# Performance work log

Measured on AMD Instinct MI355X. Metric: run time of the kernel, lower is better.

## Reference

```python
import jax, jax.numpy as jnp
import numpy as np

N = 100000   # nodes
E = 1600000  # edges (avg degree 16)
IN, HID, OUT = 128, 128, 64
EPS = 1e-5


def setup_inputs() -> dict:
    key = jax.random.key(0)
    ks = jax.random.split(key, 8)
    x = jax.random.normal(ks[0], (N, IN), dtype=jnp.float32)
    edge_index = jax.random.randint(ks[1], (2, E), 0, N, dtype=jnp.int64)

    def w(k, i, o):
        return jax.random.normal(k, (i, o), dtype=jnp.float32) / np.float32(np.sqrt(i))

    return {
        'x': x,
        'edge_index': edge_index,
        'W1': w(ks[2], IN, HID), 'b1': jnp.zeros((HID,), jnp.float32),
        'g1': jnp.ones((HID,), jnp.float32), 'be1': jnp.zeros((HID,), jnp.float32),
        'W2': w(ks[3], HID, HID), 'b2': jnp.zeros((HID,), jnp.float32),
        'g2': jnp.ones((HID,), jnp.float32), 'be2': jnp.zeros((HID,), jnp.float32),
        'W3': w(ks[4], HID, OUT), 'b3': jnp.zeros((OUT,), jnp.float32),
    }


def gcn_conv(x, W, b, src, dst, n):
    # GCNConv: x' = D^{-1/2} (A + I) D^{-1/2} X W + b
    h = x @ W                                   # [N, F_out]
    loop = jnp.arange(n, dtype=src.dtype)
    s = jnp.concatenate([src, loop])            # self-loops appended
    d = jnp.concatenate([dst, loop])
    deg = jax.ops.segment_sum(jnp.ones_like(d, dtype=h.dtype), d, num_segments=n)
    dinv = jax.lax.rsqrt(jnp.maximum(deg, 1.0))  # deg >= 1 due to self-loops
    norm = dinv[s] * dinv[d]                     # [E+N]
    out = jax.ops.segment_sum(h[s] * norm[:, None], d, num_segments=n)
    return out + b


def batch_norm(x, gamma, beta):
    m = x.mean(axis=0)
    v = x.var(axis=0)  # biased variance, as used for normalization in torch BN
    return (x - m) * jax.lax.rsqrt(v + EPS) * gamma + beta


def reference(x, edge_index, W1, b1, g1, be1, W2, b2, g2, be2, W3, b3):
    src, dst = edge_index[0], edge_index[1]
    r = x                                        # residual (skip = Identity, in_dim == hidden_dim)
    h = batch_norm(gcn_conv(x, W1, b1, src, dst, N), g1, be1) + r
    r = h
    h = jax.nn.relu(h)                           # dropout p=0 -> identity
    h = batch_norm(gcn_conv(h, W2, b2, src, dst, N), g2, be2) + r
    h = jax.nn.relu(h)
    out = gcn_conv(h, W3, b3, src, dst, N)       # last layer: no bn/skip/relu
    return out
```

## Files before the change

### kernel.cpp

```cpp
#include <hip/hip_runtime.h>

static constexpr int kN = 100000;
static constexpr int kE = 1600000;
static constexpr float kEps = 1e-5f;

static constexpr int kBSH = 9;
static constexpr int kNB = (kN + 511) >> kBSH;
static constexpr int kBCAP = 12288;
static constexpr int kCHUNK = 4096;
static constexpr int kPad = 16;

typedef __attribute__((ext_vector_type(8))) short short8;
typedef __attribute__((ext_vector_type(4))) float float4v;
typedef __attribute__((ext_vector_type(2))) float float2v;

static __device__ inline unsigned short f2bf(float f) {
  union { float f; unsigned int u; } v; v.f = f;
  unsigned int r = v.u + 0x7fffu + ((v.u >> 16) & 1u);
  return (unsigned short)(r >> 16);
}
static __device__ inline float bf2f(unsigned int bits16) {
  union { unsigned int u; float f; } v; v.u = bits16 << 16; return v.f;
}
static __device__ inline unsigned int pack2bf(float lo, float hi) {
  return (unsigned int)f2bf(lo) | ((unsigned int)f2bf(hi) << 16);
}

__global__ __launch_bounds__(512) void bin_k(const int* __restrict__ src,
                                             const int* __restrict__ dst,
                                             int* __restrict__ gcursor,
                                             int2* __restrict__ gstage) {
  __shared__ int s_cnt[256];
  __shared__ int s_scan[256];
  __shared__ int s_base[256];
  __shared__ int s_cur[256];
  __shared__ int s_gb[256];
  __shared__ int2 s_stage[kCHUNK];
  int tid = threadIdx.x;
  int e0 = blockIdx.x * kCHUNK;
  int n = kE - e0; if (n > kCHUNK) n = kCHUNK;
  if (tid < 256) s_cnt[tid] = 0;
  __syncthreads();
  for (int j = tid; j < n; j += 512) {
    atomicAdd(&s_cnt[dst[e0 + j] >> kBSH], 1);
  }
  __syncthreads();
  int v = 0;
  if (tid < 256) { v = s_cnt[tid]; s_scan[tid] = v; }
  __syncthreads();
  #pragma unroll
  for (int o = 1; o < 256; o <<= 1) {
    int t = (tid >= o && tid < 256) ? s_scan[tid - o] : 0;
    __syncthreads();
    if (tid < 256) s_scan[tid] += t;
    __syncthreads();
  }
  if (tid < 256) {
    int excl = s_scan[tid] - v;
    s_base[tid] = excl;
    s_cur[tid] = excl;
  }
  __syncthreads();
  if (tid < kNB && s_cnt[tid] > 0) s_gb[tid] = atomicAdd(&gcursor[tid], s_cnt[tid]);
  for (int j = tid; j < n; j += 512) {
    int s = src[e0 + j];
    int d = dst[e0 + j];
    int p = atomicAdd(&s_cur[d >> kBSH], 1);
    s_stage[p] = make_int2(s, d);
  }
  __syncthreads();
  for (int j = tid; j < n; j += 512) {
    int2 e = s_stage[j];
    int b = e.y >> kBSH;
    gstage[(size_t)b * kBCAP + s_gb[b] + (j - s_base[b])] = e;
  }
}

__global__ __launch_bounds__(256) void alloc_hist_k(const int2* __restrict__ gstage,
                                                    const int* __restrict__ gcursor,
                                                    int* __restrict__ counter,
                                                    int* __restrict__ deg,
                                                    int* __restrict__ row_start,
                                                    float* __restrict__ dinv) {
  __shared__ int s_deg[1 << kBSH];
  __shared__ int s_scan[256];
  __shared__ int s_bcast;
  int b = blockIdx.x, tid = threadIdx.x;
  int n0 = b << kBSH;
  s_deg[tid] = 0;
  s_deg[tid + 256] = 0;
  __syncthreads();
  int cnt = gcursor[b];
  const int2* seg = gstage + (size_t)b * kBCAP;
  for (int j = tid; j < cnt; j += 256) {
    atomicAdd(&s_deg[seg[j].y - n0], 1);
  }
  __syncthreads();
  int i0 = 2 * tid, i1 = 2 * tid + 1;
  int d0 = s_deg[i0], d1 = s_deg[i1];
  int pd0 = (d0 + kPad - 1) & ~(kPad - 1);
  int pd1 = (d1 + kPad - 1) & ~(kPad - 1);
  int sum = pd0 + pd1;
  s_scan[tid] = sum;
  __syncthreads();
  #pragma unroll
  for (int o = 1; o < 256; o <<= 1) {
    int t = (tid >= o) ? s_scan[tid - o] : 0;
    __syncthreads();
    s_scan[tid] += t;
    __syncthreads();
  }
  if (tid == 255) s_bcast = atomicAdd(counter, s_scan[255]);
  __syncthreads();
  int base = s_bcast + s_scan[tid] - sum;
  int node0 = n0 + i0, node1 = n0 + i1;
  if (node0 < kN) {
    deg[node0] = d0;
    row_start[node0] = base;
    dinv[node0] = rsqrtf((float)(d0 + 1));
  }
  if (node1 < kN) {
    deg[node1] = d1;
    row_start[node1] = base + pd0;
    dinv[node1] = rsqrtf((float)(d1 + 1));
  }
}

__global__ __launch_bounds__(256) void scatter2_k(const int2* __restrict__ gstage,
                                                  const int* __restrict__ gcursor,
                                                  const int* __restrict__ rowst,
                                                  const int* __restrict__ deg,
                                                  int* __restrict__ csr_src) {
  __shared__ int s_cur[1 << kBSH];
  int b = blockIdx.x, tid = threadIdx.x;
  int n0 = b << kBSH;
  int nn = kN - n0; if (nn > (1 << kBSH)) nn = 1 << kBSH;
  for (int i = tid; i < nn; i += 256) s_cur[i] = rowst[n0 + i];
  __syncthreads();
  int cnt = gcursor[b];
  const int2* seg = gstage + (size_t)b * kBCAP;
  for (int j = tid; j < cnt; j += 256) {
    int2 e = seg[j];
    int pos = atomicAdd(&s_cur[e.y - n0], 1);
    csr_src[pos] = e.x;
  }
  __syncthreads();
  for (int i = tid; i < nn; i += 256) {
    int d = deg[n0 + i];
    int endp = rowst[n0 + i] + ((d + kPad - 1) & ~(kPad - 1));
    for (int p = s_cur[i]; p < endp; ++p) csr_src[p] = kN;
  }
}

__global__ void convert_w_all_k(const float* __restrict__ W1, const float* __restrict__ W2,
                                const float* __restrict__ W3,
                                unsigned short* __restrict__ wf1,
                                unsigned short* __restrict__ wf2,
                                unsigned short* __restrict__ wf3,
                                unsigned char* __restrict__ hF8,
                                unsigned short* __restrict__ hH) {
  int tid = blockIdx.x * blockDim.x + threadIdx.x;
  const float* W;
  unsigned short* Wf;
  int BNO;
  if (tid < 2048) { W = W1; Wf = wf1; BNO = 128; }
  else if (tid < 4096) { W = W2; Wf = wf2; BNO = 128; tid -= 2048; }
  else if (tid < 5120) { W = W3; Wf = wf3; BNO = 64; tid -= 4096; }
  else if (tid < 5152) {
    ((unsigned int*)(hF8 + (size_t)kN * 128))[tid - 5120] = 0u;
    return;
  } else if (tid < 5184) {
    ((unsigned int*)(hH + (size_t)kN * 64))[tid - 5152] = 0u;
    return;
  } else return;
  int l = tid & 63;
  int frag = tid >> 6;
  int q = frag & 3;
  int t = frag >> 2;
  int n = t * 16 + (l & 15);
  int kbase = q * 32 + ((l >> 4) << 3);
  unsigned short v[8] __attribute__((aligned(16)));
  #pragma unroll
  for (int j = 0; j < 8; ++j) v[j] = f2bf(W[(kbase + j) * BNO + n]);
  ((uint4*)Wf)[tid] = *(const uint4*)v;
}

template <int BNO, bool AF32, bool OUT8>
__global__ __launch_bounds__(256) void gemm_mfma_k(const void* __restrict__ Aptr,
                                                   const unsigned short* __restrict__ Wf,
                                                   const float* __restrict__ dinv,
                                                   void* __restrict__ Cptr,
                                                   float* __restrict__ stats) {
  if (stats && blockIdx.x == 0) stats[threadIdx.x] = 0.f;
  int wid = (int)((blockIdx.x * blockDim.x + threadIdx.x) >> 6);
  if (wid >= kN / 16) return;
  int l = threadIdx.x & 63;
  int r0 = wid * 16;
  short8 a[4];
  if constexpr (AF32) {
    const float* Af = (const float*)Aptr + (size_t)(r0 + (l & 15)) * 128 + ((l >> 4) << 3);
    #pragma unroll
    for (int q = 0; q < 4; ++q) {
      float4 u0 = *(const float4*)(Af + q * 32);
      float4 u1 = *(const float4*)(Af + q * 32 + 4);
      short8 t;
      t[0] = (short)f2bf(u0.x); t[1] = (short)f2bf(u0.y);
      t[2] = (short)f2bf(u0.z); t[3] = (short)f2bf(u0.w);
      t[4] = (short)f2bf(u1.x); t[5] = (short)f2bf(u1.y);
      t[6] = (short)f2bf(u1.z); t[7] = (short)f2bf(u1.w);
      a[q] = t;
    }
  } else {
    const short8* Arow =
        (const short8*)((const unsigned short*)Aptr + (size_t)(r0 + (l & 15)) * 128 + ((l >> 4) << 3));
    #pragma unroll
    for (int q = 0; q < 4; ++q) a[q] = Arow[q * 4];
  }
  const short8* Wv = (const short8*)Wf + l;
  constexpr int NT = BNO / 16;
  float4v acc[NT];
  #pragma unroll
  for (int t = 0; t < NT; ++t) {
    acc[t] = (float4v){0.f, 0.f, 0.f, 0.f};
    #pragma unroll
    for (int q = 0; q < 4; ++q) {
      short8 b = Wv[(t * 4 + q) * 64];
      acc[t] = __builtin_amdgcn_mfma_f32_16x16x32_bf16(a[q], b, acc[t], 0, 0, 0);
    }
  }
  int orow = r0 + ((l >> 4) << 2);
  int ocol = l & 15;
  float dv[4];
  #pragma unroll
  for (int r = 0; r < 4; ++r) dv[r] = dinv[orow + r];
  #pragma unroll
  for (int t = 0; t < NT; ++t) {
    #pragma unroll
    for (int r = 0; r < 4; ++r) {
      float val = acc[t][r] * dv[r];
      if constexpr (OUT8) {
        unsigned int u = __builtin_amdgcn_cvt_pk_fp8_f32(val, val, 0u, false);
        ((unsigned char*)Cptr)[(size_t)(orow + r) * BNO + t * 16 + ocol] = (unsigned char)(u & 0xffu);
      } else {
        ((unsigned short*)Cptr)[(size_t)(orow + r) * BNO + t * 16 + ocol] = f2bf(val);
      }
    }
  }
}

__global__ __launch_bounds__(256) void aggregate128_k(
    const unsigned char* __restrict__ H8, const int* __restrict__ row_start,
    const int* __restrict__ deg, const int* __restrict__ csr_src,
    const float* __restrict__ dinv, const float* __restrict__ bias,
    unsigned int* __restrict__ outp, float* __restrict__ stats) {
  __shared__ float s_sum[128], s_sq[128];
  int tid = threadIdx.x;
  if (tid < 128) { s_sum[tid] = 0.f; s_sq[tid] = 0.f; }
  __syncthreads();
  int lane = tid & 63;
  int qt = lane >> 4;
  int ql = lane & 15;
  int nwaves = gridDim.x * (blockDim.x >> 6);
  int gwave = (int)((blockIdx.x * blockDim.x + tid) >> 6);
  const uint2* H2 = (const uint2*)H8;
  float4 blo = ((const float4*)bias)[2 * ql];
  float4 bhi = ((const float4*)bias)[2 * ql + 1];
  float st[8] = {0.f, 0.f, 0.f, 0.f, 0.f, 0.f, 0.f, 0.f};
  float sqa[8] = {0.f, 0.f, 0.f, 0.f, 0.f, 0.f, 0.f, 0.f};
  auto accum = [](float (&a)[8], uint2 v) {
    float2v p0 = __builtin_amdgcn_cvt_pk_f32_fp8(v.x, false);
    float2v p1 = __builtin_amdgcn_cvt_pk_f32_fp8(v.x, true);
    float2v p2 = __builtin_amdgcn_cvt_pk_f32_fp8(v.y, false);
    float2v p3 = __builtin_amdgcn_cvt_pk_f32_fp8(v.y, true);
    a[0] += p0.x; a[1] += p0.y; a[2] += p1.x; a[3] += p1.y;
    a[4] += p2.x; a[5] += p2.y; a[6] += p3.x; a[7] += p3.y;
  };
  int node = gwave;
  int rs = 0, pd = 0;
  float di = 1.f;
  int ec = kN;
  if (node < kN) {
    rs = row_start[node];
    pd = (deg[node] + kPad - 1) & ~(kPad - 1);
    di = dinv[node];
    ec = csr_src[rs + lane];
  }
  while (node < kN) {
    int cur_rs = rs, cur_pd = pd, cur_e = ec;
    float cur_di = di;
    int nxt = node + nwaves;
    if (nxt < kN) {
      rs = row_start[nxt];
      pd = (deg[nxt] + kPad - 1) & ~(kPad - 1);
      di = dinv[nxt];
      ec = csr_src[rs + lane];
    }
    float a[8] = {0.f, 0.f, 0.f, 0.f, 0.f, 0.f, 0.f, 0.f};
    uint2 vself = H2[(size_t)node * 16 + ql];
    int nb = cur_pd >> 4;
    int nb4 = nb > 4 ? 4 : nb;
    for (int i = 0; i < nb4; ++i) {
      int s[4];
      uint2 v[4];
      #pragma unroll
      for (int j = 0; j < 4; ++j) s[j] = __shfl(cur_e, i * 16 + 4 * j + qt, 64);
      #pragma unroll
      for (int j = 0; j < 4; ++j) v[j] = H2[(size_t)s[j] * 16 + ql];
      #pragma unroll
      for (int j = 0; j < 4; ++j) accum(a, v[j]);
    }
    for (int i = 4; i < nb; ++i) {
      int ee = csr_src[cur_rs + i * 16 + (lane & 15)];
      int s[4];
      uint2 v[4];
      #pragma unroll
      for (int j = 0; j < 4; ++j) s[j] = __shfl(ee, 4 * j + qt, 64);
      #pragma unroll
      for (int j = 0; j < 4; ++j) v[j] = H2[(size_t)s[j] * 16 + ql];
      #pragma unroll
      for (int j = 0; j < 4; ++j) accum(a, v[j]);
    }
    #pragma unroll
    for (int j = 0; j < 8; ++j) {
      a[j] += __shfl_xor(a[j], 16, 64);
      a[j] += __shfl_xor(a[j], 32, 64);
    }
    accum(a, vself);
    float o[8];
    o[0] = cur_di * a[0] + blo.x; o[1] = cur_di * a[1] + blo.y;
    o[2] = cur_di * a[2] + blo.z; o[3] = cur_di * a[3] + blo.w;
    o[4] = cur_di * a[4] + bhi.x; o[5] = cur_di * a[5] + bhi.y;
    o[6] = cur_di * a[6] + bhi.z; o[7] = cur_di * a[7] + bhi.w;
    if (qt == 0) {
      uint4 ov;
      ov.x = pack2bf(o[0], o[1]); ov.y = pack2bf(o[2], o[3]);
      ov.z = pack2bf(o[4], o[5]); ov.w = pack2bf(o[6], o[7]);
      ((uint4*)outp)[(size_t)node * 16 + ql] = ov;
      #pragma unroll
      for (int j = 0; j < 8; ++j) { st[j] += o[j]; sqa[j] += o[j] * o[j]; }
    }
    node = nxt;
  }
  if (qt == 0) {
    #pragma unroll
    for (int j = 0; j < 8; ++j) {
      atomicAdd(&s_sum[8 * ql + j], st[j]);
      atomicAdd(&s_sq[8 * ql + j], sqa[j]);
    }
  }
  __syncthreads();
  if (tid < 128) {
    atomicAdd(&stats[tid], s_sum[tid]);
    atomicAdd(&stats[128 + tid], s_sq[tid]);
  }
}

__global__ __launch_bounds__(256) void aggregate64_k(
    const unsigned short* __restrict__ Hb, const int* __restrict__ row_start,
    const int* __restrict__ deg, const int* __restrict__ csr_src,
    const float* __restrict__ dinv, const float* __restrict__ bias,
    float* __restrict__ outp) {
  int tid = threadIdx.x;
  int lane = tid & 63;
  int qt = lane >> 4;
  int ql = lane & 15;
  int nwaves = gridDim.x * (blockDim.x >> 6);
  int gwave = (int)((blockIdx.x * blockDim.x + tid) >> 6);
  const uint2* H2 = (const uint2*)Hb;
  float4 b4 = ((const float4*)bias)[ql];
  auto accum = [](float (&a)[4], uint2 v) {
    a[0] += bf2f(v.x & 0xffffu); a[1] += bf2f(v.x >> 16);
    a[2] += bf2f(v.y & 0xffffu); a[3] += bf2f(v.y >> 16);
  };
  int node = gwave;
  int rs = 0, pd = 0;
  float di = 1.f;
  int ec = kN;
  if (node < kN) {
    rs = row_start[node];
    pd = (deg[node] + kPad - 1) & ~(kPad - 1);
    di = dinv[node];
    ec = csr_src[rs + lane];
  }
  while (node < kN) {
    int cur_rs = rs, cur_pd = pd, cur_e = ec;
    float cur_di = di;
    int nxt = node + nwaves;
    if (nxt < kN) {
      rs = row_start[nxt];
      pd = (deg[nxt] + kPad - 1) & ~(kPad - 1);
      di = dinv[nxt];
      ec = csr_src[rs + lane];
    }
    float a[4] = {0.f, 0.f, 0.f, 0.f};
    uint2 vself = H2[(size_t)node * 16 + ql];
    int nb = cur_pd >> 4;
    int nb4 = nb > 4 ? 4 : nb;
    for (int i = 0; i < nb4; ++i) {
      int s[4];
      uint2 v[4];
      #pragma unroll
      for (int j = 0; j < 4; ++j) s[j] = __shfl(cur_e, i * 16 + 4 * j + qt, 64);
      #pragma unroll
      for (int j = 0; j < 4; ++j) v[j] = H2[(size_t)s[j] * 16 + ql];
      #pragma unroll
      for (int j = 0; j < 4; ++j) accum(a, v[j]);
    }
    for (int i = 4; i < nb; ++i) {
      int ee = csr_src[cur_rs + i * 16 + (lane & 15)];
      int s[4];
      uint2 v[4];
      #pragma unroll
      for (int j = 0; j < 4; ++j) s[j] = __shfl(ee, 4 * j + qt, 64);
      #pragma unroll
      for (int j = 0; j < 4; ++j) v[j] = H2[(size_t)s[j] * 16 + ql];
      #pragma unroll
      for (int j = 0; j < 4; ++j) accum(a, v[j]);
    }
    #pragma unroll
    for (int j = 0; j < 4; ++j) {
      a[j] += __shfl_xor(a[j], 16, 64);
      a[j] += __shfl_xor(a[j], 32, 64);
    }
    accum(a, vself);
    if (qt == 0) {
      ((float4*)outp)[(size_t)node * 16 + ql] =
          make_float4(cur_di * a[0] + b4.x, cur_di * a[1] + b4.y,
                      cur_di * a[2] + b4.z, cur_di * a[3] + b4.w);
    }
    node = nxt;
  }
}

template <bool WRITE_Z, bool RF32>
__global__ void bn_apply_res_k(const unsigned int* __restrict__ a, const void* __restrict__ rp,
                               const float* __restrict__ stats, const float* __restrict__ g,
                               const float* __restrict__ be, unsigned int* __restrict__ z,
                               unsigned int* __restrict__ rb) {
  __shared__ float lss[256];
  int t = threadIdx.x;
  if (t < 128) {
    float mean = stats[t] * (1.f / kN);
    float var = stats[128 + t] * (1.f / kN) - mean * mean;
    float inv = rsqrtf(var + kEps);
    float sc = g[t] * inv;
    lss[t] = sc;
    lss[128 + t] = be[t] - mean * sc;
  }
  __syncthreads();
  int idx = blockIdx.x * blockDim.x + t;
  if (idx >= kN * 16) return;
  uint4 av = ((const uint4*)a)[idx];
  float r[8];
  if constexpr (RF32) {
    float4 r0 = ((const float4*)rp)[idx * 2];
    float4 r1 = ((const float4*)rp)[idx * 2 + 1];
    r[0] = r0.x; r[1] = r0.y; r[2] = r0.z; r[3] = r0.w;
    r[4] = r1.x; r[5] = r1.y; r[6] = r1.z; r[7] = r1.w;
  } else {
    uint4 rv = ((const uint4*)rp)[idx];
    r[0] = bf2f(rv.x & 0xffffu); r[1] = bf2f(rv.x >> 16);
    r[2] = bf2f(rv.y & 0xffffu); r[3] = bf2f(rv.y >> 16);
    r[4] = bf2f(rv.z & 0xffffu); r[5] = bf2f(rv.z >> 16);
    r[6] = bf2f(rv.w & 0xffffu); r[7] = bf2f(rv.w >> 16);
  }
  int c = (idx & 15) * 8;
  float o[8];
  unsigned int apk[4] = {av.x, av.y, av.z, av.w};
  #pragma unroll
  for (int j = 0; j < 4; ++j) {
    o[2 * j]     = lss[c + 2 * j] * bf2f(apk[j] & 0xffffu) + lss[128 + c + 2 * j] + r[2 * j];
    o[2 * j + 1] = lss[c + 2 * j + 1] * bf2f(apk[j] >> 16) + lss[128 + c + 2 * j + 1] + r[2 * j + 1];
  }
  if (WRITE_Z) {
    uint4 zv;
    zv.x = pack2bf(o[0], o[1]); zv.y = pack2bf(o[2], o[3]);
    zv.z = pack2bf(o[4], o[5]); zv.w = pack2bf(o[6], o[7]);
    ((uint4*)z)[idx] = zv;
  }
  uint4 hv;
  hv.x = pack2bf(fmaxf(o[0], 0.f), fmaxf(o[1], 0.f));
  hv.y = pack2bf(fmaxf(o[2], 0.f), fmaxf(o[3], 0.f));
  hv.z = pack2bf(fmaxf(o[4], 0.f), fmaxf(o[5], 0.f));
  hv.w = pack2bf(fmaxf(o[6], 0.f), fmaxf(o[7], 0.f));
  ((uint4*)rb)[idx] = hv;
}

extern "C" void kernel_launch(void* const* d_in, const int* in_sizes, int n_in,
                              void* d_out, int out_size, void* d_ws, size_t ws_size,
                              hipStream_t stream) {
  const float* x   = (const float*)d_in[0];
  const int*   ei  = (const int*)d_in[1];
  const float* W1  = (const float*)d_in[2];
  const float* b1  = (const float*)d_in[3];
  const float* g1  = (const float*)d_in[4];
  const float* be1 = (const float*)d_in[5];
  const float* W2  = (const float*)d_in[6];
  const float* b2  = (const float*)d_in[7];
  const float* g2  = (const float*)d_in[8];
  const float* be2 = (const float*)d_in[9];
  const float* W3  = (const float*)d_in[10];
  const float* b3  = (const float*)d_in[11];
  float* outp = (float*)d_out;

  const int* src = ei;
  const int* dst = ei + kE;

  char* ws = (char*)d_ws;
  size_t off = 0;
  auto alloc = [&](size_t bytes) -> void* {
    void* p = ws + off;
    off = (off + bytes + 255) & ~size_t(255);
    return p;
  };
  unsigned char* hF8 = (unsigned char*)alloc((size_t)(kN + 1) * 128);
  unsigned short* hH = (unsigned short*)alloc((size_t)(kN + 1) * 64 * 2);
  unsigned int* aB = (unsigned int*)alloc((size_t)kN * 64 * 4);
  unsigned int* zC = (unsigned int*)alloc((size_t)kN * 64 * 4);
  unsigned int* hb = (unsigned int*)alloc((size_t)kN * 64 * 4);
  int*   csr_src  = (int*)alloc((size_t)(3200000 + 64) * 4);
  int2*  gstage   = (int2*)alloc((size_t)kNB * kBCAP * 8);
  int*   gcursor  = (int*)alloc((kNB + 1) * 4);
  int*   counter  = gcursor + kNB;
  int*   deg      = (int*)alloc((size_t)kN * 4);
  float* dinv     = (float*)alloc((size_t)kN * 4);
  int*   rowst    = (int*)alloc((size_t)kN * 4);
  float* stats    = (float*)alloc(256 * 4);
  unsigned short* wf1 = (unsigned short*)alloc(128 * 128 * 2);
  unsigned short* wf2 = (unsigned short*)alloc(128 * 128 * 2);
  unsigned short* wf3 = (unsigned short*)alloc(128 * 64 * 2);

  const int TB = 256;
  int blkBin = (kE + kCHUNK - 1) / kCHUNK;
  int blkGemm = (kN / 16 + 3) / 4;
  int blkApply = kN * 16 / TB;
  const int blkAgg = 2048;

  hipMemsetAsync(gcursor, 0, (kNB + 1) * 4, stream);
  bin_k<<<blkBin, 512, 0, stream>>>(src, dst, gcursor, gstage);
  alloc_hist_k<<<kNB, TB, 0, stream>>>(gstage, gcursor, counter, deg, rowst, dinv);
  scatter2_k<<<kNB, TB, 0, stream>>>(gstage, gcursor, rowst, deg, csr_src);
  convert_w_all_k<<<21, TB, 0, stream>>>(W1, W2, W3, wf1, wf2, wf3, hF8, hH);

  gemm_mfma_k<128, true, true><<<blkGemm, 256, 0, stream>>>(x, wf1, dinv, hF8, stats);
  aggregate128_k<<<blkAgg, TB, 0, stream>>>(hF8, rowst, deg, csr_src, dinv, b1, aB, stats);
  bn_apply_res_k<true, true><<<blkApply, TB, 0, stream>>>(aB, x, stats, g1, be1, zC, hb);

  gemm_mfma_k<128, false, true><<<blkGemm, 256, 0, stream>>>((const unsigned short*)hb, wf2, dinv, hF8, stats);
  aggregate128_k<<<blkAgg, TB, 0, stream>>>(hF8, rowst, deg, csr_src, dinv, b2, aB, stats);
  bn_apply_res_k<false, false><<<blkApply, TB, 0, stream>>>(aB, zC, stats, g2, be2, nullptr, hb);

  gemm_mfma_k<64, false, false><<<blkGemm, 256, 0, stream>>>((const unsigned short*)hb, wf3, dinv, hH, nullptr);
  aggregate64_k<<<blkAgg, TB, 0, stream>>>(hH, rowst, deg, csr_src, dinv, b3, outp);
}
```

Measured before the change: 423.8 us.

## Split gathered features into column quarters mapped to XCD pairs for aggregation

```diff
diff --git a/kernel.cpp b/kernel.cpp
--- a/kernel.cpp
+++ b/kernel.cpp
@@ -10,9 +10,12 @@
 static constexpr int kCHUNK = 4096;
 static constexpr int kPad = 16;
 
+static constexpr size_t kQStride = (size_t)(kN + 1) * 32;
+
 typedef __attribute__((ext_vector_type(8))) short short8;
 typedef __attribute__((ext_vector_type(4))) float float4v;
 typedef __attribute__((ext_vector_type(2))) float float2v;
+typedef __attribute__((ext_vector_type(4))) unsigned int uint4v;
 
 static __device__ inline unsigned short f2bf(float f) {
   union { float f; unsigned int u; } v; v.f = f;
@@ -167,10 +170,14 @@
   else if (tid < 4096) { W = W2; Wf = wf2; BNO = 128; tid -= 2048; }
   else if (tid < 5120) { W = W3; Wf = wf3; BNO = 64; tid -= 4096; }
   else if (tid < 5152) {
-    ((unsigned int*)(hF8 + (size_t)kN * 128))[tid - 5120] = 0u;
+    int k = tid - 5120;
+    unsigned int* p = (unsigned int*)(hF8 + (size_t)(k >> 3) * kQStride + (size_t)kN * 32);
+    p[k & 7] = 0u;
     return;
   } else if (tid < 5184) {
-    ((unsigned int*)(hH + (size_t)kN * 64))[tid - 5152] = 0u;
+    int k = tid - 5152;
+    unsigned int* p = (unsigned int*)((unsigned char*)hH + (size_t)(k >> 3) * kQStride + (size_t)kN * 32);
+    p[k & 7] = 0u;
     return;
   } else return;
   int l = tid & 63;
@@ -238,11 +245,14 @@
     #pragma unroll
     for (int r = 0; r < 4; ++r) {
       float val = acc[t][r] * dv[r];
+      int c = t * 16 + ocol;
       if constexpr (OUT8) {
         unsigned int u = __builtin_amdgcn_cvt_pk_fp8_f32(val, val, 0u, false);
-        ((unsigned char*)Cptr)[(size_t)(orow + r) * BNO + t * 16 + ocol] = (unsigned char)(u & 0xffu);
+        unsigned char* p = (unsigned char*)Cptr + (size_t)(c >> 5) * kQStride;
+        p[(size_t)(orow + r) * 32 + (c & 31)] = (unsigned char)(u & 0xffu);
       } else {
-        ((unsigned short*)Cptr)[(size_t)(orow + r) * BNO + t * 16 + ocol] = f2bf(val);
+        unsigned short* p = (unsigned short*)((unsigned char*)Cptr + (size_t)(c >> 4) * kQStride);
+        p[(size_t)(orow + r) * 16 + (c & 15)] = f2bf(val);
       }
     }
   }
@@ -258,94 +268,101 @@
   if (tid < 128) { s_sum[tid] = 0.f; s_sq[tid] = 0.f; }
   __syncthreads();
   int lane = tid & 63;
-  int qt = lane >> 4;
-  int ql = lane & 15;
-  int nwaves = gridDim.x * (blockDim.x >> 6);
-  int gwave = (int)((blockIdx.x * blockDim.x + tid) >> 6);
-  const uint2* H2 = (const uint2*)H8;
-  float4 blo = ((const float4*)bias)[2 * ql];
-  float4 bhi = ((const float4*)bias)[2 * ql + 1];
+  int ql = lane & 3;
+  int qt = (lane >> 2) & 3;
+  int nsub = lane >> 4;
+  int xcd = blockIdx.x & 7;
+  int q = xcd >> 1;
+  int lb = ((blockIdx.x >> 3) << 1) | (xcd & 1);
+  int gw = lb * 4 + (tid >> 6);
+  constexpr int GW = 2048;
+  constexpr int NBATCH = kN / 4;
+  const uint2* H2 = (const uint2*)(H8 + (size_t)q * kQStride);
+  float4 blo = ((const float4*)bias)[q * 8 + ql * 2];
+  float4 bhi = ((const float4*)bias)[q * 8 + ql * 2 + 1];
   float st[8] = {0.f, 0.f, 0.f, 0.f, 0.f, 0.f, 0.f, 0.f};
   float sqa[8] = {0.f, 0.f, 0.f, 0.f, 0.f, 0.f, 0.f, 0.f};
-  auto accum = [](float (&a)[8], uint2 v) {
-    float2v p0 = __builtin_amdgcn_cvt_pk_f32_fp8(v.x, false);
-    float2v p1 = __builtin_amdgcn_cvt_pk_f32_fp8(v.x, true);
-    float2v p2 = __builtin_amdgcn_cvt_pk_f32_fp8(v.y, false);
-    float2v p3 = __builtin_amdgcn_cvt_pk_f32_fp8(v.y, true);
-    a[0] += p0.x; a[1] += p0.y; a[2] += p1.x; a[3] += p1.y;
-    a[4] += p2.x; a[5] += p2.y; a[6] += p3.x; a[7] += p3.y;
+  auto accum = [](float2v (&a)[4], uint2 v) {
+    a[0] += __builtin_amdgcn_cvt_pk_f32_fp8(v.x, false);
+    a[1] += __builtin_amdgcn_cvt_pk_f32_fp8(v.x, true);
+    a[2] += __builtin_amdgcn_cvt_pk_f32_fp8(v.y, false);
+    a[3] += __builtin_amdgcn_cvt_pk_f32_fp8(v.y, true);
   };
-  int node = gwave;
-  int rs = 0, pd = 0;
+  int batch = gw;
+  int node = 0, rs = 0, pd = 0, e0 = kN, e1 = kN;
   float di = 1.f;
-  int ec = kN;
-  if (node < kN) {
-    rs = row_start[node];
-    pd = (deg[node] + kPad - 1) & ~(kPad - 1);
-    di = dinv[node];
-    ec = csr_src[rs + lane];
-  }
-  while (node < kN) {
-    int cur_rs = rs, cur_pd = pd, cur_e = ec;
-    float cur_di = di;
-    int nxt = node + nwaves;
-    if (nxt < kN) {
-      rs = row_start[nxt];
-      pd = (deg[nxt] + kPad - 1) & ~(kPad - 1);
-      di = dinv[nxt];
-      ec = csr_src[rs + lane];
-    }
-    float a[8] = {0.f, 0.f, 0.f, 0.f, 0.f, 0.f, 0.f, 0.f};
-    uint2 vself = H2[(size_t)node * 16 + ql];
-    int nb = cur_pd >> 4;
-    int nb4 = nb > 4 ? 4 : nb;
-    for (int i = 0; i < nb4; ++i) {
+  auto loadmeta = [&](int b, int& node_, int& rs_, int& pd_, float& di_, int& e0_, int& e1_) {
+    node_ = b * 4 + nsub;
+    rs_ = __builtin_nontemporal_load(row_start + node_);
+    int dg = __builtin_nontemporal_load(deg + node_);
+    pd_ = (dg + kPad - 1) & ~(kPad - 1);
+    di_ = __builtin_nontemporal_load(dinv + node_);
+    e0_ = __builtin_nontemporal_load(csr_src + rs_ + (lane & 15));
+    e1_ = kN;
+    if (pd_ > 16) e1_ = __builtin_nontemporal_load(csr_src + rs_ + 16 + (lane & 15));
+  };
+  if (batch < NBATCH) loadmeta(batch, node, rs, pd, di, e0, e1);
+  while (batch < NBATCH) {
+    int cn = node, crs = rs, cpd = pd, ce0 = e0, ce1 = e1;
+    float cdi = di;
+    int nb = batch + GW;
+    if (nb < NBATCH) loadmeta(nb, node, rs, pd, di, e0, e1);
+    uint2 vself = H2[(size_t)cn * 4 + ql];
+    float2v a[4] = {{0.f, 0.f}, {0.f, 0.f}, {0.f, 0.f}, {0.f, 0.f}};
+    int pm = cpd;
+    { int t1 = __shfl_xor(pm, 16, 64); pm = pm < t1 ? t1 : pm;
+      int t2 = __shfl_xor(pm, 32, 64); pm = pm < t2 ? t2 : pm; }
+    int ng = pm >> 4;
+    auto gather16 = [&](int eg, int g) {
       int s[4];
+      #pragma unroll
+      for (int i = 0; i < 4; ++i) {
+        int se = __shfl(eg, (lane & 48) + i * 4 + qt, 64);
+        s[i] = (g * 16 + i * 4 + qt < cpd) ? se : kN;
+      }
       uint2 v[4];
       #pragma unroll
-      for (int j = 0; j < 4; ++j) s[j] = __shfl(cur_e, i * 16 + 4 * j + qt, 64);
-      #pragma unroll
-      for (int j = 0; j < 4; ++j) v[j] = H2[(size_t)s[j] * 16 + ql];
-      #pragma unroll
-      for (int j = 0; j < 4; ++j) accum(a, v[j]);
-    }
-    for (int i = 4; i < nb; ++i) {
-      int ee = csr_src[cur_rs + i * 16 + (lane & 15)];
-      int s[4];
-      uint2 v[4];
-      #pragma unroll
-      for (int j = 0; j < 4; ++j) s[j] = __shfl(ee, 4 * j + qt, 64);
-      #pragma unroll
-      for (int j = 0; j < 4; ++j) v[j] = H2[(size_t)s[j] * 16 + ql];
-      #pragma unroll
-      for (int j = 0; j < 4; ++j) accum(a, v[j]);
-    }
+      for (int i = 0; i < 4; ++i) v[i] = H2[(size_t)s[i] * 4 + ql];
+      #pragma unroll
+      for (int i = 0; i < 4; ++i) accum(a, v[i]);
+    };
+    if (ng > 0) gather16(ce0, 0);
+    if (ng > 1) gather16(ce1, 1);
+    for (int g = 2; g < ng; ++g) {
+      int ee = kN;
+      if (cpd > g * 16) ee = __builtin_nontemporal_load(csr_src + crs + g * 16 + (lane & 15));
+      gather16(ee, g);
+    }
+    #pragma unroll
+    for (int j = 0; j < 4; ++j) {
+      float2v t;
+      t.x = __shfl_xor(a[j].x, 4, 64); t.y = __shfl_xor(a[j].y, 4, 64);
+      a[j] += t;
+      t.x = __shfl_xor(a[j].x, 8, 64); t.y = __shfl_xor(a[j].y, 8, 64);
+      a[j] += t;
+    }
+    accum(a, vself);
+    if (qt == 0) {
+      float o[8];
+      o[0] = cdi * a[0].x + blo.x; o[1] = cdi * a[0].y + blo.y;
+      o[2] = cdi * a[1].x + blo.z; o[3] = cdi * a[1].y + blo.w;
+      o[4] = cdi * a[2].x + bhi.x; o[5] = cdi * a[2].y + bhi.y;
+      o[6] = cdi * a[3].x + bhi.z; o[7] = cdi * a[3].y + bhi.w;
+      uint4v ov;
+      ov[0] = pack2bf(o[0], o[1]); ov[1] = pack2bf(o[2], o[3]);
+      ov[2] = pack2bf(o[4], o[5]); ov[3] = pack2bf(o[6], o[7]);
+      __builtin_nontemporal_store(ov, (uint4v*)outp + (size_t)cn * 16 + q * 4 + ql);
+      #pragma unroll
+      for (int j = 0; j < 8; ++j) { st[j] += o[j]; sqa[j] += o[j] * o[j]; }
+    }
+    batch = nb;
+  }
+  if (qt == 0) {
+    int c0 = q * 32 + ql * 8;
     #pragma unroll
     for (int j = 0; j < 8; ++j) {
-      a[j] += __shfl_xor(a[j], 16, 64);
-      a[j] += __shfl_xor(a[j], 32, 64);
-    }
-    accum(a, vself);
-    float o[8];
-    o[0] = cur_di * a[0] + blo.x; o[1] = cur_di * a[1] + blo.y;
-    o[2] = cur_di * a[2] + blo.z; o[3] = cur_di * a[3] + blo.w;
-    o[4] = cur_di * a[4] + bhi.x; o[5] = cur_di * a[5] + bhi.y;
-    o[6] = cur_di * a[6] + bhi.z; o[7] = cur_di * a[7] + bhi.w;
-    if (qt == 0) {
-      uint4 ov;
-      ov.x = pack2bf(o[0], o[1]); ov.y = pack2bf(o[2], o[3]);
-      ov.z = pack2bf(o[4], o[5]); ov.w = pack2bf(o[6], o[7]);
-      ((uint4*)outp)[(size_t)node * 16 + ql] = ov;
-      #pragma unroll
-      for (int j = 0; j < 8; ++j) { st[j] += o[j]; sqa[j] += o[j] * o[j]; }
-    }
-    node = nxt;
-  }
-  if (qt == 0) {
-    #pragma unroll
-    for (int j = 0; j < 8; ++j) {
-      atomicAdd(&s_sum[8 * ql + j], st[j]);
-      atomicAdd(&s_sq[8 * ql + j], sqa[j]);
+      atomicAdd(&s_sum[c0 + j], st[j]);
+      atomicAdd(&s_sq[c0 + j], sqa[j]);
     }
   }
   __syncthreads();
@@ -362,73 +379,85 @@
     float* __restrict__ outp) {
   int tid = threadIdx.x;
   int lane = tid & 63;
-  int qt = lane >> 4;
-  int ql = lane & 15;
-  int nwaves = gridDim.x * (blockDim.x >> 6);
-  int gwave = (int)((blockIdx.x * blockDim.x + tid) >> 6);
-  const uint2* H2 = (const uint2*)Hb;
-  float4 b4 = ((const float4*)bias)[ql];
-  auto accum = [](float (&a)[4], uint2 v) {
-    a[0] += bf2f(v.x & 0xffffu); a[1] += bf2f(v.x >> 16);
-    a[2] += bf2f(v.y & 0xffffu); a[3] += bf2f(v.y >> 16);
+  int ql = lane & 3;
+  int qt = (lane >> 2) & 3;
+  int nsub = lane >> 4;
+  int xcd = blockIdx.x & 7;
+  int q = xcd >> 1;
+  int lb = ((blockIdx.x >> 3) << 1) | (xcd & 1);
+  int gw = lb * 4 + (tid >> 6);
+  constexpr int GW = 2048;
+  constexpr int NBATCH = kN / 4;
+  const uint2* H2 = (const uint2*)((const unsigned char*)Hb + (size_t)q * kQStride);
+  float4 b4 = ((const float4*)bias)[q * 4 + ql];
+  auto accum = [](float2v (&a)[2], uint2 v) {
+    union { unsigned int u; float f; } w0, w1, w2, w3;
+    w0.u = v.x << 16; w1.u = v.x & 0xffff0000u;
+    w2.u = v.y << 16; w3.u = v.y & 0xffff0000u;
+    a[0].x += w0.f; a[0].y += w1.f;
+    a[1].x += w2.f; a[1].y += w3.f;
   };
-  int node = gwave;
-  int rs = 0, pd = 0;
+  int batch = gw;
+  int node = 0, rs = 0, pd = 0, e0 = kN, e1 = kN;
   float di = 1.f;
-  int ec = kN;
-  if (node < kN) {
-    rs = row_start[node];
-    pd = (deg[node] + kPad - 1) & ~(kPad - 1);
-    di = dinv[node];
-    ec = csr_src[rs + lane];
-  }
-  while (node < kN) {
-    int cur_rs = rs, cur_pd = pd, cur_e = ec;
-    float cur_di = di;
-    int nxt = node + nwaves;
-    if (nxt < kN) {
-      rs = row_start[nxt];
-      pd = (deg[nxt] + kPad - 1) & ~(kPad - 1);
-      di = dinv[nxt];
-      ec = csr_src[rs + lane];
-    }
-    float a[4] = {0.f, 0.f, 0.f, 0.f};
-    uint2 vself = H2[(size_t)node * 16 + ql];
-    int nb = cur_pd >> 4;
-    int nb4 = nb > 4 ? 4 : nb;
-    for (int i = 0; i < nb4; ++i) {
+  auto loadmeta = [&](int b, int& node_, int& rs_, int& pd_, float& di_, int& e0_, int& e1_) {
+    node_ = b * 4 + nsub;
+    rs_ = __builtin_nontemporal_load(row_start + node_);
+    int dg = __builtin_nontemporal_load(deg + node_);
+    pd_ = (dg + kPad - 1) & ~(kPad - 1);
+    di_ = __builtin_nontemporal_load(dinv + node_);
+    e0_ = __builtin_nontemporal_load(csr_src + rs_ + (lane & 15));
+    e1_ = kN;
+    if (pd_ > 16) e1_ = __builtin_nontemporal_load(csr_src + rs_ + 16 + (lane & 15));
+  };
+  if (batch < NBATCH) loadmeta(batch, node, rs, pd, di, e0, e1);
+  while (batch < NBATCH) {
+    int cn = node, crs = rs, cpd = pd, ce0 = e0, ce1 = e1;
+    float cdi = di;
+    int nb = batch + GW;
+    if (nb < NBATCH) loadmeta(nb, node, rs, pd, di, e0, e1);
+    uint2 vself = H2[(size_t)cn * 4 + ql];
+    float2v a[2] = {{0.f, 0.f}, {0.f, 0.f}};
+    int pm = cpd;
+    { int t1 = __shfl_xor(pm, 16, 64); pm = pm < t1 ? t1 : pm;
+      int t2 = __shfl_xor(pm, 32, 64); pm = pm < t2 ? t2 : pm; }
+    int ng = pm >> 4;
+    auto gather16 = [&](int eg, int g) {
       int s[4];
+      #pragma unroll
+      for (int i = 0; i < 4; ++i) {
+        int se = __shfl(eg, (lane & 48) + i * 4 + qt, 64);
+        s[i] = (g * 16 + i * 4 + qt < cpd) ? se : kN;
+      }
       uint2 v[4];
       #pragma unroll
-      for (int j = 0; j < 4; ++j) s[j] = __shfl(cur_e, i * 16 + 4 * j + qt, 64);
-      #pragma unroll
-      for (int j = 0; j < 4; ++j) v[j] = H2[(size_t)s[j] * 16 + ql];
-      #pragma unroll
-      for (int j = 0; j < 4; ++j) accum(a, v[j]);
-    }
-    for (int i = 4; i < nb; ++i) {
-      int ee = csr_src[cur_rs + i * 16 + (lane & 15)];
-      int s[4];
-      uint2 v[4];
-      #pragma unroll
-      for (int j = 0; j < 4; ++j) s[j] = __shfl(ee, 4 * j + qt, 64);
-      #pragma unroll
-      for (int j = 0; j < 4; ++j) v[j] = H2[(size_t)s[j] * 16 + ql];
-      #pragma unroll
-      for (int j = 0; j < 4; ++j) accum(a, v[j]);
-    }
-    #pragma unroll
-    for (int j = 0; j < 4; ++j) {
-      a[j] += __shfl_xor(a[j], 16, 64);
-      a[j] += __shfl_xor(a[j], 32, 64);
+      for (int i = 0; i < 4; ++i) v[i] = H2[(size_t)s[i] * 4 + ql];
+      #pragma unroll
+      for (int i = 0; i < 4; ++i) accum(a, v[i]);
+    };
+    if (ng > 0) gather16(ce0, 0);
+    if (ng > 1) gather16(ce1, 1);
+    for (int g = 2; g < ng; ++g) {
+      int ee = kN;
+      if (cpd > g * 16) ee = __builtin_nontemporal_load(csr_src + crs + g * 16 + (lane & 15));
+      gather16(ee, g);
+    }
+    #pragma unroll
+    for (int j = 0; j < 2; ++j) {
+      float2v t;
+      t.x = __shfl_xor(a[j].x, 4, 64); t.y = __shfl_xor(a[j].y, 4, 64);
+      a[j] += t;
+      t.x = __shfl_xor(a[j].x, 8, 64); t.y = __shfl_xor(a[j].y, 8, 64);
+      a[j] += t;
     }
     accum(a, vself);
     if (qt == 0) {
-      ((float4*)outp)[(size_t)node * 16 + ql] =
-          make_float4(cur_di * a[0] + b4.x, cur_di * a[1] + b4.y,
-                      cur_di * a[2] + b4.z, cur_di * a[3] + b4.w);
-    }
-    node = nxt;
+      float4v ov;
+      ov[0] = cdi * a[0].x + b4.x; ov[1] = cdi * a[0].y + b4.y;
+      ov[2] = cdi * a[1].x + b4.z; ov[3] = cdi * a[1].y + b4.w;
+      __builtin_nontemporal_store(ov, (float4v*)outp + (size_t)cn * 16 + q * 4 + ql);
+    }
+    batch = nb;
   }
 }
 
@@ -513,8 +542,8 @@
     off = (off + bytes + 255) & ~size_t(255);
     return p;
   };
-  unsigned char* hF8 = (unsigned char*)alloc((size_t)(kN + 1) * 128);
-  unsigned short* hH = (unsigned short*)alloc((size_t)(kN + 1) * 64 * 2);
+  unsigned char* hF8 = (unsigned char*)alloc(4 * kQStride);
+  unsigned short* hH = (unsigned short*)alloc(4 * kQStride);
   unsigned int* aB = (unsigned int*)alloc((size_t)kN * 64 * 4);
   unsigned int* zC = (unsigned int*)alloc((size_t)kN * 64 * 4);
   unsigned int* hb = (unsigned int*)alloc((size_t)kN * 64 * 4);
```

Result: slower. 537.2 us (+26.8%).

## Batch four nodes per wave in aggregation to raise gather memory parallelism

Applied to the files above, without the earlier changes.

```diff
diff --git a/kernel.cpp b/kernel.cpp
--- a/kernel.cpp
+++ b/kernel.cpp
@@ -275,71 +275,100 @@
     a[0] += p0.x; a[1] += p0.y; a[2] += p1.x; a[3] += p1.y;
     a[4] += p2.x; a[5] += p2.y; a[6] += p3.x; a[7] += p3.y;
   };
-  int node = gwave;
-  int rs = 0, pd = 0;
-  float di = 1.f;
-  int ec = kN;
-  if (node < kN) {
-    rs = row_start[node];
-    pd = (deg[node] + kPad - 1) & ~(kPad - 1);
-    di = dinv[node];
-    ec = csr_src[rs + lane];
-  }
-  while (node < kN) {
-    int cur_rs = rs, cur_pd = pd, cur_e = ec;
-    float cur_di = di;
-    int nxt = node + nwaves;
-    if (nxt < kN) {
-      rs = row_start[nxt];
-      pd = (deg[nxt] + kPad - 1) & ~(kPad - 1);
-      di = dinv[nxt];
-      ec = csr_src[rs + lane];
-    }
-    float a[8] = {0.f, 0.f, 0.f, 0.f, 0.f, 0.f, 0.f, 0.f};
-    uint2 vself = H2[(size_t)node * 16 + ql];
-    int nb = cur_pd >> 4;
-    int nb4 = nb > 4 ? 4 : nb;
-    for (int i = 0; i < nb4; ++i) {
-      int s[4];
-      uint2 v[4];
-      #pragma unroll
-      for (int j = 0; j < 4; ++j) s[j] = __shfl(cur_e, i * 16 + 4 * j + qt, 64);
-      #pragma unroll
-      for (int j = 0; j < 4; ++j) v[j] = H2[(size_t)s[j] * 16 + ql];
-      #pragma unroll
-      for (int j = 0; j < 4; ++j) accum(a, v[j]);
-    }
-    for (int i = 4; i < nb; ++i) {
-      int ee = csr_src[cur_rs + i * 16 + (lane & 15)];
-      int s[4];
-      uint2 v[4];
-      #pragma unroll
-      for (int j = 0; j < 4; ++j) s[j] = __shfl(ee, 4 * j + qt, 64);
-      #pragma unroll
-      for (int j = 0; j < 4; ++j) v[j] = H2[(size_t)s[j] * 16 + ql];
-      #pragma unroll
-      for (int j = 0; j < 4; ++j) accum(a, v[j]);
-    }
-    #pragma unroll
-    for (int j = 0; j < 8; ++j) {
-      a[j] += __shfl_xor(a[j], 16, 64);
-      a[j] += __shfl_xor(a[j], 32, 64);
-    }
-    accum(a, vself);
-    float o[8];
-    o[0] = cur_di * a[0] + blo.x; o[1] = cur_di * a[1] + blo.y;
-    o[2] = cur_di * a[2] + blo.z; o[3] = cur_di * a[3] + blo.w;
-    o[4] = cur_di * a[4] + bhi.x; o[5] = cur_di * a[5] + bhi.y;
-    o[6] = cur_di * a[6] + bhi.z; o[7] = cur_di * a[7] + bhi.w;
-    if (qt == 0) {
-      uint4 ov;
-      ov.x = pack2bf(o[0], o[1]); ov.y = pack2bf(o[2], o[3]);
-      ov.z = pack2bf(o[4], o[5]); ov.w = pack2bf(o[6], o[7]);
-      ((uint4*)outp)[(size_t)node * 16 + ql] = ov;
-      #pragma unroll
-      for (int j = 0; j < 8; ++j) { st[j] += o[j]; sqa[j] += o[j] * o[j]; }
-    }
-    node = nxt;
+  constexpr int NBATCH = kN / 4;
+  int prs[4], ppd[4], pe[4];
+  float pdi[4];
+  auto loadbatch = [&](int b) {
+    #pragma unroll
+    for (int j = 0; j < 4; ++j) {
+      int nd = b * 4 + j;
+      prs[j] = row_start[nd];
+      int dg = deg[nd];
+      ppd[j] = (dg + kPad - 1) & ~(kPad - 1);
+      pdi[j] = dinv[nd];
+      pe[j] = csr_src[prs[j] + lane];
+    }
+  };
+  int batch = gwave;
+  if (batch < NBATCH) loadbatch(batch);
+  while (batch < NBATCH) {
+    int crs[4], cpd[4], ce[4];
+    float cdi[4];
+    #pragma unroll
+    for (int j = 0; j < 4; ++j) {
+      crs[j] = prs[j]; cpd[j] = ppd[j]; cdi[j] = pdi[j]; ce[j] = pe[j];
+    }
+    int nxt = batch + nwaves;
+    if (nxt < NBATCH) loadbatch(nxt);
+    uint2 vs[4], g0[4][4], g1[4][4];
+    #pragma unroll
+    for (int j = 0; j < 4; ++j) {
+      vs[j] = H2[(size_t)(batch * 4 + j) * 16 + ql];
+      #pragma unroll
+      for (int i = 0; i < 4; ++i) {
+        int s0 = __shfl(ce[j], 4 * i + qt, 64);
+        s0 = (cpd[j] > 0) ? s0 : kN;
+        g0[j][i] = H2[(size_t)s0 * 16 + ql];
+      }
+      #pragma unroll
+      for (int i = 0; i < 4; ++i) {
+        int s1 = __shfl(ce[j], 16 + 4 * i + qt, 64);
+        s1 = (cpd[j] >= 32) ? s1 : kN;
+        g1[j][i] = H2[(size_t)s1 * 16 + ql];
+      }
+    }
+    #pragma unroll
+    for (int j = 0; j < 4; ++j) {
+      int cn = batch * 4 + j;
+      float a[8] = {0.f, 0.f, 0.f, 0.f, 0.f, 0.f, 0.f, 0.f};
+      #pragma unroll
+      for (int i = 0; i < 4; ++i) accum(a, g0[j][i]);
+      #pragma unroll
+      for (int i = 0; i < 4; ++i) accum(a, g1[j][i]);
+      int nb = cpd[j] >> 4;
+      int nb4 = nb < 4 ? nb : 4;
+      for (int g = 2; g < nb4; ++g) {
+        int s[4];
+        uint2 v[4];
+        #pragma unroll
+        for (int i = 0; i < 4; ++i) s[i] = __shfl(ce[j], g * 16 + 4 * i + qt, 64);
+        #pragma unroll
+        for (int i = 0; i < 4; ++i) v[i] = H2[(size_t)s[i] * 16 + ql];
+        #pragma unroll
+        for (int i = 0; i < 4; ++i) accum(a, v[i]);
+      }
+      for (int g = 4; g < nb; ++g) {
+        int ee = csr_src[crs[j] + g * 16 + (lane & 15)];
+        int s[4];
+        uint2 v[4];
+        #pragma unroll
+        for (int i = 0; i < 4; ++i) s[i] = __shfl(ee, 4 * i + qt, 64);
+        #pragma unroll
+        for (int i = 0; i < 4; ++i) v[i] = H2[(size_t)s[i] * 16 + ql];
+        #pragma unroll
+        for (int i = 0; i < 4; ++i) accum(a, v[i]);
+      }
+      #pragma unroll
+      for (int k = 0; k < 8; ++k) {
+        a[k] += __shfl_xor(a[k], 16, 64);
+        a[k] += __shfl_xor(a[k], 32, 64);
+      }
+      accum(a, vs[j]);
+      if (qt == 0) {
+        float o[8];
+        o[0] = cdi[j] * a[0] + blo.x; o[1] = cdi[j] * a[1] + blo.y;
+        o[2] = cdi[j] * a[2] + blo.z; o[3] = cdi[j] * a[3] + blo.w;
+        o[4] = cdi[j] * a[4] + bhi.x; o[5] = cdi[j] * a[5] + bhi.y;
+        o[6] = cdi[j] * a[6] + bhi.z; o[7] = cdi[j] * a[7] + bhi.w;
+        uint4 ov;
+        ov.x = pack2bf(o[0], o[1]); ov.y = pack2bf(o[2], o[3]);
+        ov.z = pack2bf(o[4], o[5]); ov.w = pack2bf(o[6], o[7]);
+        ((uint4*)outp)[(size_t)cn * 16 + ql] = ov;
+        #pragma unroll
+        for (int k = 0; k < 8; ++k) { st[k] += o[k]; sqa[k] += o[k] * o[k]; }
+      }
+    }
+    batch = nxt;
   }
   if (qt == 0) {
     #pragma unroll
@@ -372,63 +401,92 @@
     a[0] += bf2f(v.x & 0xffffu); a[1] += bf2f(v.x >> 16);
     a[2] += bf2f(v.y & 0xffffu); a[3] += bf2f(v.y >> 16);
   };
-  int node = gwave;
-  int rs = 0, pd = 0;
-  float di = 1.f;
-  int ec = kN;
-  if (node < kN) {
-    rs = row_start[node];
-    pd = (deg[node] + kPad - 1) & ~(kPad - 1);
-    di = dinv[node];
-    ec = csr_src[rs + lane];
-  }
-  while (node < kN) {
-    int cur_rs = rs, cur_pd = pd, cur_e = ec;
-    float cur_di = di;
-    int nxt = node + nwaves;
-    if (nxt < kN) {
-      rs = row_start[nxt];
-      pd = (deg[nxt] + kPad - 1) & ~(kPad - 1);
-      di = dinv[nxt];
-      ec = csr_src[rs + lane];
-    }
-    float a[4] = {0.f, 0.f, 0.f, 0.f};
-    uint2 vself = H2[(size_t)node * 16 + ql];
-    int nb = cur_pd >> 4;
-    int nb4 = nb > 4 ? 4 : nb;
-    for (int i = 0; i < nb4; ++i) {
-      int s[4];
-      uint2 v[4];
-      #pragma unroll
-      for (int j = 0; j < 4; ++j) s[j] = __shfl(cur_e, i * 16 + 4 * j + qt, 64);
-      #pragma unroll
-      for (int j = 0; j < 4; ++j) v[j] = H2[(size_t)s[j] * 16 + ql];
-      #pragma unroll
-      for (int j = 0; j < 4; ++j) accum(a, v[j]);
-    }
-    for (int i = 4; i < nb; ++i) {
-      int ee = csr_src[cur_rs + i * 16 + (lane & 15)];
-      int s[4];
-      uint2 v[4];
-      #pragma unroll
-      for (int j = 0; j < 4; ++j) s[j] = __shfl(ee, 4 * j + qt, 64);
-      #pragma unroll
-      for (int j = 0; j < 4; ++j) v[j] = H2[(size_t)s[j] * 16 + ql];
-      #pragma unroll
-      for (int j = 0; j < 4; ++j) accum(a, v[j]);
-    }
-    #pragma unroll
-    for (int j = 0; j < 4; ++j) {
-      a[j] += __shfl_xor(a[j], 16, 64);
-      a[j] += __shfl_xor(a[j], 32, 64);
-    }
-    accum(a, vself);
-    if (qt == 0) {
-      ((float4*)outp)[(size_t)node * 16 + ql] =
-          make_float4(cur_di * a[0] + b4.x, cur_di * a[1] + b4.y,
-                      cur_di * a[2] + b4.z, cur_di * a[3] + b4.w);
-    }
-    node = nxt;
+  constexpr int NBATCH = kN / 4;
+  int prs[4], ppd[4], pe[4];
+  float pdi[4];
+  auto loadbatch = [&](int b) {
+    #pragma unroll
+    for (int j = 0; j < 4; ++j) {
+      int nd = b * 4 + j;
+      prs[j] = row_start[nd];
+      int dg = deg[nd];
+      ppd[j] = (dg + kPad - 1) & ~(kPad - 1);
+      pdi[j] = dinv[nd];
+      pe[j] = csr_src[prs[j] + lane];
+    }
+  };
+  int batch = gwave;
+  if (batch < NBATCH) loadbatch(batch);
+  while (batch < NBATCH) {
+    int crs[4], cpd[4], ce[4];
+    float cdi[4];
+    #pragma unroll
+    for (int j = 0; j < 4; ++j) {
+      crs[j] = prs[j]; cpd[j] = ppd[j]; cdi[j] = pdi[j]; ce[j] = pe[j];
+    }
+    int nxt = batch + nwaves;
+    if (nxt < NBATCH) loadbatch(nxt);
+    uint2 vs[4], g0[4][4], g1[4][4];
+    #pragma unroll
+    for (int j = 0; j < 4; ++j) {
+      vs[j] = H2[(size_t)(batch * 4 + j) * 16 + ql];
+      #pragma unroll
+      for (int i = 0; i < 4; ++i) {
+        int s0 = __shfl(ce[j], 4 * i + qt, 64);
+        s0 = (cpd[j] > 0) ? s0 : kN;
+        g0[j][i] = H2[(size_t)s0 * 16 + ql];
+      }
+      #pragma unroll
+      for (int i = 0; i < 4; ++i) {
+        int s1 = __shfl(ce[j], 16 + 4 * i + qt, 64);
+        s1 = (cpd[j] >= 32) ? s1 : kN;
+        g1[j][i] = H2[(size_t)s1 * 16 + ql];
+      }
+    }
+    #pragma unroll
+    for (int j = 0; j < 4; ++j) {
+      int cn = batch * 4 + j;
+      float a[4] = {0.f, 0.f, 0.f, 0.f};
+      #pragma unroll
+      for (int i = 0; i < 4; ++i) accum(a, g0[j][i]);
+      #pragma unroll
+      for (int i = 0; i < 4; ++i) accum(a, g1[j][i]);
+      int nb = cpd[j] >> 4;
+      int nb4 = nb < 4 ? nb : 4;
+      for (int g = 2; g < nb4; ++g) {
+        int s[4];
+        uint2 v[4];
+        #pragma unroll
+        for (int i = 0; i < 4; ++i) s[i] = __shfl(ce[j], g * 16 + 4 * i + qt, 64);
+        #pragma unroll
+        for (int i = 0; i < 4; ++i) v[i] = H2[(size_t)s[i] * 16 + ql];
+        #pragma unroll
+        for (int i = 0; i < 4; ++i) accum(a, v[i]);
+      }
+      for (int g = 4; g < nb; ++g) {
+        int ee = csr_src[crs[j] + g * 16 + (lane & 15)];
+        int s[4];
+        uint2 v[4];
+        #pragma unroll
+        for (int i = 0; i < 4; ++i) s[i] = __shfl(ee, 4 * i + qt, 64);
+        #pragma unroll
+        for (int i = 0; i < 4; ++i) v[i] = H2[(size_t)s[i] * 16 + ql];
+        #pragma unroll
+        for (int i = 0; i < 4; ++i) accum(a, v[i]);
+      }
+      #pragma unroll
+      for (int k = 0; k < 4; ++k) {
+        a[k] += __shfl_xor(a[k], 16, 64);
+        a[k] += __shfl_xor(a[k], 32, 64);
+      }
+      accum(a, vs[j]);
+      if (qt == 0) {
+        ((float4*)outp)[(size_t)cn * 16 + ql] =
+            make_float4(cdi[j] * a[0] + b4.x, cdi[j] * a[1] + b4.y,
+                        cdi[j] * a[2] + b4.z, cdi[j] * a[3] + b4.w);
+      }
+    }
+    batch = nxt;
   }
 }
 
@@ -534,7 +592,7 @@
   int blkBin = (kE + kCHUNK - 1) / kCHUNK;
   int blkGemm = (kN / 16 + 3) / 4;
   int blkApply = kN * 16 / TB;
-  const int blkAgg = 2048;
+  const int blkAgg = 1568;
 
   hipMemsetAsync(gcursor, 0, (kNB + 1) * 4, stream);
   bin_k<<<blkBin, 512, 0, stream>>>(src, dst, gcursor, gstage);
```

Result: slower. 435.7 us (+2.8%).
